# Optimization experiments

Measured on AMD Instinct MI355X. Metric: run time of the kernel, lower is better.

Reference implementation:

```python
import jax, jax.numpy as jnp
import numpy as np

B, A, D = 32, 1024, 128
THR = 0.05  # proximity_threshold


def setup_inputs() -> dict:
    key = jax.random.key(0)
    k1, k2, k3, k4, k5 = jax.random.split(key, 5)
    s = 1.0 / np.sqrt(D)
    return {
        "agent_embeds": jax.random.normal(k1, (B, A, D), jnp.float32),
        "agent_coords": jax.random.uniform(k2, (B, A, 2), jnp.float32),
        "agent_mask": jax.random.randint(k3, (B, A), 0, 2).astype(jnp.int32),
        "W1": (jax.random.normal(k4, (D, D), jnp.float32) * s),
        "b1": jnp.zeros((D,), jnp.float32),
        "W2": (jax.random.normal(k5, (D, D), jnp.float32) * s),
        "b2": jnp.zeros((D,), jnp.float32),
    }


def _cluster(coords, valid):
    """Greedy sequential proximity clustering (same order/semantics as the torch loop).
    coords [A,2], valid [A] bool -> assigned [A] int32 (group id; invalid agents = -2)."""
    diff = coords[:, None, :] - coords[None, :, :]          # [A,A,2]
    near_all = jnp.sum(diff * diff, axis=-1) < (THR * THR)   # dist < thr  <=>  dist^2 < thr^2
    assigned0 = jnp.where(valid, -1, -2).astype(jnp.int32)

    def step(carry, i):
        assigned, gid = carry
        start = assigned[i] == -1                 # valid and not yet assigned -> new group
        take = start & near_all[i] & (assigned == -1)  # includes i (dist ii = 0)
        assigned = jnp.where(take, gid, assigned)
        gid = gid + start.astype(jnp.int32)
        return (assigned, gid), None

    (assigned, _), _ = jax.lax.scan(step, (assigned0, jnp.int32(0)), jnp.arange(A))
    return assigned


def reference(agent_embeds, agent_coords, agent_mask, W1, b1, W2, b2):
    valid = agent_mask.astype(bool)                          # [B,A]
    assigned = jax.vmap(_cluster)(agent_coords, valid)       # [B,A] int32

    w = valid.astype(agent_embeds.dtype)                     # [B,A]
    seg = jnp.where(valid, assigned, 0)                      # invalid -> seg 0 with weight 0

    def pool(emb, sg, wt):  # per batch: segment-mean into at most A groups (padded)
        sums = jax.ops.segment_sum(emb * wt[:, None], sg, num_segments=A)  # [A,D]
        cnt = jax.ops.segment_sum(wt, sg, num_segments=A)                  # [A]
        return sums / jnp.maximum(cnt, 1.0)[:, None], cnt > 0

    group_tokens, group_mask = jax.vmap(pool)(agent_embeds, seg, w)  # [B,A,D], [B,A]

    # group_proj MLP applied to the whole (zero-padded) token tensor, as in torch
    h = jax.nn.gelu(group_tokens @ W1 + b1, approximate=False)
    group_tokens = h @ W2 + b2

    agent_to_group = jnp.where(valid, assigned, -1)
    return group_tokens, group_mask, agent_to_group
```

## Files before the change

kernel.cpp:

```cpp
#include <hip/hip_runtime.h>
#include <hip/hip_bf16.h>

#define NB 32
#define NA 1024
#define ND 128
#define TG 16

__device__ __forceinline__ float gelu_exact(float x) {
    return 0.5f * x * (1.0f + erff(x * 0.7071067811865476f));
}

__global__ __launch_bounds__(1024, 1) void fused_kernel(
    const float2* __restrict__ coords, const int* __restrict__ mask,
    const float* __restrict__ emb,
    int* __restrict__ gcount, float* __restrict__ tokens,
    float* __restrict__ out_mask, float* __restrict__ out_a2g,
    const float* __restrict__ b1, const float* __restrict__ W2,
    const float* __restrict__ b2, float* __restrict__ empty_row)
{
    __shared__ float2 ring[NA + 4];
    __shared__ int cnt_s[NA];
    __shared__ int bufA[NA];
    __shared__ int bufB[NA];
    __shared__ int memb[NA];
    __shared__ int done_s[16];
    __shared__ int lead_cnt;

    const int tid = threadIdx.x;

    if (blockIdx.x == NB) {
        float* hbuf = (float*)ring;
        if (tid < ND) hbuf[tid] = gelu_exact(b1[tid]);
        __syncthreads();
        if (tid < ND) {
            float acc = b2[tid];
            for (int k = 0; k < ND; ++k) acc += hbuf[k] * W2[k * ND + tid];
            empty_row[tid] = acc;
        }
        return;
    }

    const int b = blockIdx.x;
    const int w = tid >> 6;
    const int lane = tid & 63;

    if (tid < 16) done_s[tid] = -1;
    if (tid == 0) lead_cnt = 0;

    float2 p = coords[(b << 10) + tid];
    const bool valid = mask[(b << 10) + tid] != 0;
    int asg = valid ? -1 : -2;
    bool alive = valid;
    const float thr2 = 0.05f * 0.05f;

    __syncthreads();

    int seen = 0;
    int target = (w == 0) ? 0 : -1;

    while (true) {
        int c = __hip_atomic_load(&lead_cnt, __ATOMIC_ACQUIRE,
                                  __HIP_MEMORY_SCOPE_WORKGROUP);
        while (seen < c) {
            float2 l0 = ring[seen];
            float2 l1 = ring[seen + 1];
            float2 l2 = ring[seen + 2];
            float2 l3 = ring[seen + 3];
            {
                float dx = p.x - l0.x, dy = p.y - l0.y;
                float d2 = __fadd_rn(__fmul_rn(dx, dx), __fmul_rn(dy, dy));
                if (alive && d2 < thr2) { asg = seen; alive = false; }
            }
            if (seen + 1 < c) {
                float dx = p.x - l1.x, dy = p.y - l1.y;
                float d2 = __fadd_rn(__fmul_rn(dx, dx), __fmul_rn(dy, dy));
                if (alive && d2 < thr2) { asg = seen + 1; alive = false; }
            }
            if (seen + 2 < c) {
                float dx = p.x - l2.x, dy = p.y - l2.y;
                float d2 = __fadd_rn(__fmul_rn(dx, dx), __fmul_rn(dy, dy));
                if (alive && d2 < thr2) { asg = seen + 2; alive = false; }
            }
            if (seen + 3 < c) {
                float dx = p.x - l3.x, dy = p.y - l3.y;
                float d2 = __fadd_rn(__fmul_rn(dx, dx), __fmul_rn(dy, dy));
                if (alive && d2 < thr2) { asg = seen + 3; alive = false; }
            }
            seen = (seen + 4 < c) ? seen + 4 : c;
        }
        if (target < 0)
            target = __hip_atomic_load(&done_s[w - 1], __ATOMIC_ACQUIRE,
                                       __HIP_MEMORY_SCOPE_WORKGROUP);
        if (target >= 0 && seen >= target) break;
        __builtin_amdgcn_s_sleep(1);
    }

    __builtin_amdgcn_s_setprio(1);
    unsigned long long bal;
    while ((bal = __ballot(alive)) != 0ULL) {
        const int L = (int)__builtin_ctzll(bal);
        const float lx = __builtin_bit_cast(float,
            __builtin_amdgcn_readlane(__builtin_bit_cast(int, p.x), L));
        const float ly = __builtin_bit_cast(float,
            __builtin_amdgcn_readlane(__builtin_bit_cast(int, p.y), L));
        float dx = p.x - lx, dy = p.y - ly;
        float d2 = __fadd_rn(__fmul_rn(dx, dx), __fmul_rn(dy, dy));
        bool take = alive && (d2 < thr2);
        if (take) { asg = seen; alive = false; }
        if (lane == 0) {
            ring[seen] = make_float2(lx, ly);
            __hip_atomic_store(&lead_cnt, seen + 1, __ATOMIC_RELEASE,
                               __HIP_MEMORY_SCOPE_WORKGROUP);
        }
        ++seen;
    }
    __builtin_amdgcn_s_setprio(0);
    if (lane == 0)
        __hip_atomic_store(&done_s[w], seen, __ATOMIC_RELEASE,
                           __HIP_MEMORY_SCOPE_WORKGROUP);

    __syncthreads();
    const int G = lead_cnt;

    cnt_s[tid] = 0;
    __syncthreads();
    if (asg >= 0) atomicAdd(&cnt_s[asg], 1);
    __syncthreads();

    bufA[tid] = cnt_s[tid];
    __syncthreads();
    int* src = bufA;
    int* dst = bufB;
    for (int d = 1; d < NA; d <<= 1) {
        int v = src[tid];
        if (tid >= d) v += src[tid - d];
        dst[tid] = v;
        __syncthreads();
        int* tswap = src; src = dst; dst = tswap;
    }
    const int excl = src[tid] - cnt_s[tid];
    bufB[tid] = excl;
    bufA[tid] = excl;
    __syncthreads();
    if (asg >= 0) {
        int ppos = atomicAdd(&bufA[asg], 1);
        memb[ppos] = tid;
    }
    __syncthreads();

    out_a2g[(b << 10) + tid] = (asg == -2) ? -1.0f : (float)asg;
    out_mask[(b << 10) + tid] = (tid < G) ? 1.0f : 0.0f;
    if (tid == 0) gcount[b] = G;

    const int Gpad = (G + TG - 1) & ~(TG - 1);
    const float* eb = emb + ((size_t)(b) << 10) * ND;
    float* tb = tokens + ((size_t)(b) << 10) * ND;
    for (int g = w; g < Gpad; g += 16) {
        float a0 = 0.0f, a1 = 0.0f;
        if (g < G) {
            const int n = cnt_s[g];
            const int off = bufB[g];
            for (int k = 0; k < n; ++k) {
                const int a = memb[off + k];
                const float* ea = eb + (size_t)a * ND;
                a0 += ea[lane];
                a1 += ea[lane + 64];
            }
            const float den = fmaxf((float)n, 1.0f);
            a0 /= den; a1 /= den;
        }
        tb[(size_t)g * ND + lane] = a0;
        tb[(size_t)g * ND + lane + 64] = a1;
    }
}

__global__ __launch_bounds__(256, 2) void mlp_kernel(
    const float* __restrict__ tokens, const int* __restrict__ gcount,
    const float* __restrict__ empty_row,
    const float4* __restrict__ W1, const float* __restrict__ b1,
    const float4* __restrict__ W2, const float* __restrict__ b2,
    float* __restrict__ out0)
{
    const int b = blockIdx.y;
    const int g0 = blockIdx.x * TG;
    const int tid = threadIdx.x;
    float* ob = out0 + ((size_t)(b << 10) + g0) * ND;

    if (g0 >= gcount[b]) {
        float4 r = ((const float4*)empty_row)[tid & 31];
        float4* ob4 = (float4*)ob;
        ob4[tid] = r;
        ob4[tid + 256] = r;
        return;
    }

    __shared__ float4 Wl[4096];
    __shared__ float tok[TG][ND];

    {
        const float4* tsrc = (const float4*)(tokens + ((size_t)(b << 10) + g0) * ND);
        float4* tdst = (float4*)&tok[0][0];
        tdst[tid] = tsrc[tid];
        tdst[tid + 256] = tsrc[tid + 256];
    }
#pragma unroll
    for (int i = 0; i < 16; ++i) Wl[tid + i * 256] = W1[tid + i * 256];
    __syncthreads();

    const int jq = tid & 31;
    const int gs = tid >> 5;
    float acc[2][4];
#pragma unroll
    for (int jj = 0; jj < 4; ++jj) { acc[0][jj] = 0.0f; acc[1][jj] = 0.0f; }

#pragma unroll 4
    for (int dd = 0; dd < ND; ++dd) {
        float4 wv = Wl[dd * 32 + jq];
        float t0 = tok[gs][dd];
        float t1 = tok[gs + 8][dd];
        acc[0][0] += t0 * wv.x; acc[0][1] += t0 * wv.y;
        acc[0][2] += t0 * wv.z; acc[0][3] += t0 * wv.w;
        acc[1][0] += t1 * wv.x; acc[1][1] += t1 * wv.y;
        acc[1][2] += t1 * wv.z; acc[1][3] += t1 * wv.w;
    }
    float4 bb = ((const float4*)b1)[jq];
    __syncthreads();
    {
        float4 h;
        h.x = gelu_exact(acc[0][0] + bb.x);
        h.y = gelu_exact(acc[0][1] + bb.y);
        h.z = gelu_exact(acc[0][2] + bb.z);
        h.w = gelu_exact(acc[0][3] + bb.w);
        *(float4*)&tok[gs][jq * 4] = h;
        h.x = gelu_exact(acc[1][0] + bb.x);
        h.y = gelu_exact(acc[1][1] + bb.y);
        h.z = gelu_exact(acc[1][2] + bb.z);
        h.w = gelu_exact(acc[1][3] + bb.w);
        *(float4*)&tok[gs + 8][jq * 4] = h;
    }
#pragma unroll
    for (int i = 0; i < 16; ++i) Wl[tid + i * 256] = W2[tid + i * 256];
    __syncthreads();

#pragma unroll
    for (int jj = 0; jj < 4; ++jj) { acc[0][jj] = 0.0f; acc[1][jj] = 0.0f; }
#pragma unroll 4
    for (int dd = 0; dd < ND; ++dd) {
        float4 wv = Wl[dd * 32 + jq];
        float t0 = tok[gs][dd];
        float t1 = tok[gs + 8][dd];
        acc[0][0] += t0 * wv.x; acc[0][1] += t0 * wv.y;
        acc[0][2] += t0 * wv.z; acc[0][3] += t0 * wv.w;
        acc[1][0] += t1 * wv.x; acc[1][1] += t1 * wv.y;
        acc[1][2] += t1 * wv.z; acc[1][3] += t1 * wv.w;
    }
    float4 cbv = ((const float4*)b2)[jq];
    {
        float4 o;
        o.x = acc[0][0] + cbv.x; o.y = acc[0][1] + cbv.y;
        o.z = acc[0][2] + cbv.z; o.w = acc[0][3] + cbv.w;
        *(float4*)&ob[(size_t)gs * ND + jq * 4] = o;
        o.x = acc[1][0] + cbv.x; o.y = acc[1][1] + cbv.y;
        o.z = acc[1][2] + cbv.z; o.w = acc[1][3] + cbv.w;
        *(float4*)&ob[(size_t)(gs + 8) * ND + jq * 4] = o;
    }
}

extern "C" void kernel_launch(void* const* d_in, const int* in_sizes, int n_in,
                              void* d_out, int out_size, void* d_ws, size_t ws_size,
                              hipStream_t stream) {
    const float* emb    = (const float*)d_in[0];
    const float* coords = (const float*)d_in[1];
    const int*   mask   = (const int*)d_in[2];
    const float* W1     = (const float*)d_in[3];
    const float* b1     = (const float*)d_in[4];
    const float* W2     = (const float*)d_in[5];
    const float* b2     = (const float*)d_in[6];

    float* out0 = (float*)d_out;
    float* out1 = out0 + (size_t)NB * NA * ND;
    float* out2 = out1 + (size_t)NB * NA;

    float* ws_tok   = (float*)d_ws;
    int*   ws_gcnt  = (int*)(ws_tok + (size_t)NB * NA * ND);
    float* ws_empty = (float*)(ws_gcnt + NB);

    fused_kernel<<<NB + 1, 1024, 0, stream>>>(
        (const float2*)coords, mask, emb,
        ws_gcnt, ws_tok, out1, out2,
        b1, W2, b2, ws_empty);
    mlp_kernel<<<dim3(NA / TG, NB), 256, 0, stream>>>(
        ws_tok, ws_gcnt, ws_empty,
        (const float4*)W1, b1, (const float4*)W2, b2, out0);
}
```

Baseline: 147.7 us.

## Replace sequential greedy clustering with parallel neighbor-list fixpoint and fuse pooling into MLP

Each agent now builds a list of up to 16 lower-indexed neighbors in shared memory. Leader/follower status is then resolved by iterating synchronous rounds until no agent is undecided, which replaces the serialized leader-discovery loop of the greedy clustering. Segment-mean pooling moves from the clustering kernel into the MLP kernel: membership lists go through workspace and each MLP block gathers its own group tokens. The MLP also reads W1/W2 straight from global memory instead of staging them in LDS. The risks are the round count on long dependency chains, a brute-force fallback for agents with more than 16 neighbors, and uncached weight reads in the inner loop.

```diff
diff --git a/kernel.cpp b/kernel.cpp
--- a/kernel.cpp
+++ b/kernel.cpp
@@ -5,31 +5,38 @@
 #define NA 1024
 #define ND 128
 #define TG 16
+#define KNB 16
 
 __device__ __forceinline__ float gelu_exact(float x) {
     return 0.5f * x * (1.0f + erff(x * 0.7071067811865476f));
 }
 
+__device__ __forceinline__ float dist2(float ax, float ay, float bx, float by) {
+    float dx = ax - bx, dy = ay - by;
+    return __fadd_rn(__fmul_rn(dx, dx), __fmul_rn(dy, dy));
+}
+
 __global__ __launch_bounds__(1024, 1) void fused_kernel(
     const float2* __restrict__ coords, const int* __restrict__ mask,
-    const float* __restrict__ emb,
-    int* __restrict__ gcount, float* __restrict__ tokens,
+    int* __restrict__ gcount, int* __restrict__ memb_ws,
+    int* __restrict__ goff_ws, float* __restrict__ gcntf_ws,
     float* __restrict__ out_mask, float* __restrict__ out_a2g,
     const float* __restrict__ b1, const float* __restrict__ W2,
     const float* __restrict__ b2, float* __restrict__ empty_row)
 {
-    __shared__ float2 ring[NA + 4];
-    __shared__ int cnt_s[NA];
-    __shared__ int bufA[NA];
-    __shared__ int bufB[NA];
-    __shared__ int memb[NA];
-    __shared__ int done_s[16];
-    __shared__ int lead_cnt;
+    __shared__ __align__(16) float2 xy[NA];
+    __shared__ int   stat[NA];
+    __shared__ short nbr[NA * KNB];
+    __shared__ int   bufA[NA];
+    __shared__ int   bufB[NA];
+    __shared__ int   membs[NA];
+    __shared__ int   cnts[NA];
+    __shared__ int   undec_cnt;
 
     const int tid = threadIdx.x;
 
     if (blockIdx.x == NB) {
-        float* hbuf = (float*)ring;
+        float* hbuf = (float*)xy;
         if (tid < ND) hbuf[tid] = gelu_exact(b1[tid]);
         __syncthreads();
         if (tid < ND) {
@@ -41,142 +48,146 @@
     }
 
     const int b = blockIdx.x;
-    const int w = tid >> 6;
-    const int lane = tid & 63;
-
-    if (tid < 16) done_s[tid] = -1;
-    if (tid == 0) lead_cnt = 0;
-
-    float2 p = coords[(b << 10) + tid];
+    const float2 praw = coords[(b << 10) + tid];
     const bool valid = mask[(b << 10) + tid] != 0;
-    int asg = valid ? -1 : -2;
-    bool alive = valid;
+    const float2 p = valid ? praw : make_float2(1e30f, 1e30f);
+    xy[tid] = p;
+    int st = valid ? 0 : 2;
+    stat[tid] = st;
+    if (tid == 0) undec_cnt = 0;
+    __syncthreads();
+
     const float thr2 = 0.05f * 0.05f;
 
-    __syncthreads();
-
-    int seen = 0;
-    int target = (w == 0) ? 0 : -1;
-
-    while (true) {
-        int c = __hip_atomic_load(&lead_cnt, __ATOMIC_ACQUIRE,
-                                  __HIP_MEMORY_SCOPE_WORKGROUP);
-        while (seen < c) {
-            float2 l0 = ring[seen];
-            float2 l1 = ring[seen + 1];
-            float2 l2 = ring[seen + 2];
-            float2 l3 = ring[seen + 3];
-            {
-                float dx = p.x - l0.x, dy = p.y - l0.y;
-                float d2 = __fadd_rn(__fmul_rn(dx, dx), __fmul_rn(dy, dy));
-                if (alive && d2 < thr2) { asg = seen; alive = false; }
+    int nst = 0;
+    bool heavy = false;
+    {
+        const float4* xy4 = (const float4*)xy;
+        const int np2 = tid >> 1;
+        for (int j2 = 0; j2 < np2; ++j2) {
+            float4 two = xy4[j2];
+            const int j0 = j2 * 2;
+            float da = dist2(p.x, p.y, two.x, two.y);
+            float db = dist2(p.x, p.y, two.z, two.w);
+            if (da < thr2) { if (nst < KNB) nbr[tid * KNB + nst++] = (short)j0; else heavy = true; }
+            if (db < thr2) { if (nst < KNB) nbr[tid * KNB + nst++] = (short)(j0 + 1); else heavy = true; }
+        }
+        if (tid & 1) {
+            float2 q = xy[tid - 1];
+            float dc = dist2(p.x, p.y, q.x, q.y);
+            if (dc < thr2) { if (nst < KNB) nbr[tid * KNB + nst++] = (short)(tid - 1); else heavy = true; }
+        }
+    }
+    __syncthreads();
+
+    for (int round = 0; round < 4096; ++round) {
+        if (st == 0) {
+            bool anyL = false, anyU = false;
+            if (!heavy) {
+                for (int k = 0; k < nst; ++k) {
+                    int s = stat[(int)nbr[tid * KNB + k]];
+                    anyL |= (s == 1);
+                    anyU |= (s == 0);
+                }
+            } else {
+                for (int j = 0; j < tid; ++j) {
+                    float2 q = xy[j];
+                    if (dist2(p.x, p.y, q.x, q.y) < thr2) {
+                        int s = stat[j];
+                        anyL |= (s == 1);
+                        anyU |= (s == 0);
+                    }
+                }
             }
-            if (seen + 1 < c) {
-                float dx = p.x - l1.x, dy = p.y - l1.y;
-                float d2 = __fadd_rn(__fmul_rn(dx, dx), __fmul_rn(dy, dy));
-                if (alive && d2 < thr2) { asg = seen + 1; alive = false; }
+            if (anyL)       { st = 2; stat[tid] = 2; }
+            else if (!anyU) { st = 1; stat[tid] = 1; }
+        }
+        __syncthreads();
+        unsigned long long um = __ballot(st == 0);
+        if ((tid & 63) == 0 && um != 0ULL)
+            atomicAdd(&undec_cnt, (int)__popcll(um));
+        __syncthreads();
+        const int u = undec_cnt;
+        __syncthreads();
+        if (tid == 0) undec_cnt = 0;
+        if (u == 0) break;
+    }
+
+    int leader = -1;
+    if (st == 2 && valid) {
+        if (!heavy) {
+            for (int k = 0; k < nst; ++k) {
+                int j = (int)nbr[tid * KNB + k];
+                if (stat[j] == 1) { leader = j; break; }
             }
-            if (seen + 2 < c) {
-                float dx = p.x - l2.x, dy = p.y - l2.y;
-                float d2 = __fadd_rn(__fmul_rn(dx, dx), __fmul_rn(dy, dy));
-                if (alive && d2 < thr2) { asg = seen + 2; alive = false; }
+        } else {
+            for (int j = 0; j < tid; ++j) {
+                float2 q = xy[j];
+                if (dist2(p.x, p.y, q.x, q.y) < thr2 && stat[j] == 1) { leader = j; break; }
             }
-            if (seen + 3 < c) {
-                float dx = p.x - l3.x, dy = p.y - l3.y;
-                float d2 = __fadd_rn(__fmul_rn(dx, dx), __fmul_rn(dy, dy));
-                if (alive && d2 < thr2) { asg = seen + 3; alive = false; }
-            }
-            seen = (seen + 4 < c) ? seen + 4 : c;
-        }
-        if (target < 0)
-            target = __hip_atomic_load(&done_s[w - 1], __ATOMIC_ACQUIRE,
-                                       __HIP_MEMORY_SCOPE_WORKGROUP);
-        if (target >= 0 && seen >= target) break;
-        __builtin_amdgcn_s_sleep(1);
-    }
-
-    __builtin_amdgcn_s_setprio(1);
-    unsigned long long bal;
-    while ((bal = __ballot(alive)) != 0ULL) {
-        const int L = (int)__builtin_ctzll(bal);
-        const float lx = __builtin_bit_cast(float,
-            __builtin_amdgcn_readlane(__builtin_bit_cast(int, p.x), L));
-        const float ly = __builtin_bit_cast(float,
-            __builtin_amdgcn_readlane(__builtin_bit_cast(int, p.y), L));
-        float dx = p.x - lx, dy = p.y - ly;
-        float d2 = __fadd_rn(__fmul_rn(dx, dx), __fmul_rn(dy, dy));
-        bool take = alive && (d2 < thr2);
-        if (take) { asg = seen; alive = false; }
-        if (lane == 0) {
-            ring[seen] = make_float2(lx, ly);
-            __hip_atomic_store(&lead_cnt, seen + 1, __ATOMIC_RELEASE,
-                               __HIP_MEMORY_SCOPE_WORKGROUP);
-        }
-        ++seen;
-    }
-    __builtin_amdgcn_s_setprio(0);
-    if (lane == 0)
-        __hip_atomic_store(&done_s[w], seen, __ATOMIC_RELEASE,
-                           __HIP_MEMORY_SCOPE_WORKGROUP);
-
-    __syncthreads();
-    const int G = lead_cnt;
-
-    cnt_s[tid] = 0;
-    __syncthreads();
-    if (asg >= 0) atomicAdd(&cnt_s[asg], 1);
-    __syncthreads();
-
-    bufA[tid] = cnt_s[tid];
-    __syncthreads();
-    int* src = bufA;
-    int* dst = bufB;
-    for (int d = 1; d < NA; d <<= 1) {
-        int v = src[tid];
-        if (tid >= d) v += src[tid - d];
-        dst[tid] = v;
-        __syncthreads();
-        int* tswap = src; src = dst; dst = tswap;
-    }
-    const int excl = src[tid] - cnt_s[tid];
+        }
+    }
+
+    bufA[tid] = (st == 1) ? 1 : 0;
+    __syncthreads();
+    {
+        int* src = bufA; int* dst = bufB;
+        for (int d = 1; d < NA; d <<= 1) {
+            int v = src[tid];
+            if (tid >= d) v += src[tid - d];
+            dst[tid] = v;
+            __syncthreads();
+            int* t = src; src = dst; dst = t;
+        }
+    }
+    const int G = bufA[NA - 1];
+    const int mygid = bufA[tid] - ((st == 1) ? 1 : 0);
+    stat[tid] = mygid;
+    __syncthreads();
+
+    int asg;
+    if (!valid) asg = -2;
+    else if (st == 1) asg = mygid;
+    else asg = (leader >= 0) ? stat[leader] : 0;
+
+    cnts[tid] = 0;
+    membs[tid] = 0;
+    __syncthreads();
+    if (asg >= 0) atomicAdd(&cnts[asg], 1);
+    __syncthreads();
+    bufA[tid] = cnts[tid];
+    __syncthreads();
+    {
+        int* src = bufA; int* dst = bufB;
+        for (int d = 1; d < NA; d <<= 1) {
+            int v = src[tid];
+            if (tid >= d) v += src[tid - d];
+            dst[tid] = v;
+            __syncthreads();
+            int* t = src; src = dst; dst = t;
+        }
+    }
+    const int excl = bufA[tid] - cnts[tid];
+    goff_ws[(b << 10) + tid]  = excl;
+    gcntf_ws[(b << 10) + tid] = (float)cnts[tid];
     bufB[tid] = excl;
-    bufA[tid] = excl;
     __syncthreads();
     if (asg >= 0) {
-        int ppos = atomicAdd(&bufA[asg], 1);
-        memb[ppos] = tid;
-    }
-    __syncthreads();
-
+        int pos = atomicAdd(&bufB[asg], 1);
+        membs[pos] = tid;
+    }
+    __syncthreads();
+
+    memb_ws[(b << 10) + tid] = membs[tid];
     out_a2g[(b << 10) + tid] = (asg == -2) ? -1.0f : (float)asg;
     out_mask[(b << 10) + tid] = (tid < G) ? 1.0f : 0.0f;
     if (tid == 0) gcount[b] = G;
-
-    const int Gpad = (G + TG - 1) & ~(TG - 1);
-    const float* eb = emb + ((size_t)(b) << 10) * ND;
-    float* tb = tokens + ((size_t)(b) << 10) * ND;
-    for (int g = w; g < Gpad; g += 16) {
-        float a0 = 0.0f, a1 = 0.0f;
-        if (g < G) {
-            const int n = cnt_s[g];
-            const int off = bufB[g];
-            for (int k = 0; k < n; ++k) {
-                const int a = memb[off + k];
-                const float* ea = eb + (size_t)a * ND;
-                a0 += ea[lane];
-                a1 += ea[lane + 64];
-            }
-            const float den = fmaxf((float)n, 1.0f);
-            a0 /= den; a1 /= den;
-        }
-        tb[(size_t)g * ND + lane] = a0;
-        tb[(size_t)g * ND + lane + 64] = a1;
-    }
-}
-
-__global__ __launch_bounds__(256, 2) void mlp_kernel(
-    const float* __restrict__ tokens, const int* __restrict__ gcount,
-    const float* __restrict__ empty_row,
+}
+
+__global__ __launch_bounds__(256) void mlp_kernel(
+    const float* __restrict__ emb, const int* __restrict__ memb,
+    const int* __restrict__ goff, const float* __restrict__ gcntf,
+    const int* __restrict__ gcount, const float* __restrict__ empty_row,
     const float4* __restrict__ W1, const float* __restrict__ b1,
     const float4* __restrict__ W2, const float* __restrict__ b2,
     float* __restrict__ out0)
@@ -194,17 +205,27 @@
         return;
     }
 
-    __shared__ float4 Wl[4096];
     __shared__ float tok[TG][ND];
 
     {
-        const float4* tsrc = (const float4*)(tokens + ((size_t)(b << 10) + g0) * ND);
-        float4* tdst = (float4*)&tok[0][0];
-        tdst[tid] = tsrc[tid];
-        tdst[tid + 256] = tsrc[tid + 256];
-    }
-#pragma unroll
-    for (int i = 0; i < 16; ++i) Wl[tid + i * 256] = W1[tid + i * 256];
+        const int gl = tid >> 4;
+        const int sub = tid & 15;
+        const int gi = (b << 10) + g0 + gl;
+        const int n = (int)gcntf[gi];
+        const int off = goff[gi];
+        const int* mb = memb + (b << 10) + off;
+        float a0=0,a1=0,a2=0,a3=0,a4=0,a5=0,a6=0,a7=0;
+        for (int k = 0; k < n; ++k) {
+            const int a = mb[k];
+            const float4* e4 = (const float4*)(emb + ((size_t)(b << 10) + a) * ND + sub * 8);
+            float4 v0 = e4[0], v1 = e4[1];
+            a0 += v0.x; a1 += v0.y; a2 += v0.z; a3 += v0.w;
+            a4 += v1.x; a5 += v1.y; a6 += v1.z; a7 += v1.w;
+        }
+        const float den = fmaxf((float)n, 1.0f);
+        *(float4*)&tok[gl][sub * 8]     = make_float4(a0/den, a1/den, a2/den, a3/den);
+        *(float4*)&tok[gl][sub * 8 + 4] = make_float4(a4/den, a5/den, a6/den, a7/den);
+    }
     __syncthreads();
 
     const int jq = tid & 31;
@@ -215,7 +236,7 @@
 
 #pragma unroll 4
     for (int dd = 0; dd < ND; ++dd) {
-        float4 wv = Wl[dd * 32 + jq];
+        float4 wv = W1[dd * 32 + jq];
         float t0 = tok[gs][dd];
         float t1 = tok[gs + 8][dd];
         acc[0][0] += t0 * wv.x; acc[0][1] += t0 * wv.y;
@@ -238,15 +259,13 @@
         h.w = gelu_exact(acc[1][3] + bb.w);
         *(float4*)&tok[gs + 8][jq * 4] = h;
     }
-#pragma unroll
-    for (int i = 0; i < 16; ++i) Wl[tid + i * 256] = W2[tid + i * 256];
     __syncthreads();
 
 #pragma unroll
     for (int jj = 0; jj < 4; ++jj) { acc[0][jj] = 0.0f; acc[1][jj] = 0.0f; }
 #pragma unroll 4
     for (int dd = 0; dd < ND; ++dd) {
-        float4 wv = Wl[dd * 32 + jq];
+        float4 wv = W2[dd * 32 + jq];
         float t0 = tok[gs][dd];
         float t1 = tok[gs + 8][dd];
         acc[0][0] += t0 * wv.x; acc[0][1] += t0 * wv.y;
@@ -281,15 +300,17 @@
     float* out1 = out0 + (size_t)NB * NA * ND;
     float* out2 = out1 + (size_t)NB * NA;
 
-    float* ws_tok   = (float*)d_ws;
-    int*   ws_gcnt  = (int*)(ws_tok + (size_t)NB * NA * ND);
+    int*   ws_memb  = (int*)d_ws;
+    int*   ws_goff  = ws_memb + (size_t)NB * NA;
+    float* ws_gcntf = (float*)(ws_goff + (size_t)NB * NA);
+    int*   ws_gcnt  = (int*)(ws_gcntf + (size_t)NB * NA);
     float* ws_empty = (float*)(ws_gcnt + NB);
 
     fused_kernel<<<NB + 1, 1024, 0, stream>>>(
-        (const float2*)coords, mask, emb,
-        ws_gcnt, ws_tok, out1, out2,
-        b1, W2, b2, ws_empty);
+        (const float2*)coords, mask,
+        ws_gcnt, ws_memb, ws_goff, ws_gcntf,
+        out1, out2, b1, W2, b2, ws_empty);
     mlp_kernel<<<dim3(NA / TG, NB), 256, 0, stream>>>(
-        ws_tok, ws_gcnt, ws_empty,
+        emb, ws_memb, ws_goff, ws_gcntf, ws_gcnt, ws_empty,
         (const float4*)W1, b1, (const float4*)W2, b2, out0);
 }
```

Measured after the change: 232.6 us. 1.58x slower.
